# Performance work log

Hardware: AMD Instinct MI355X
Metric: run time of the kernel (lower is better)

## Reference

```python
import math
import jax, jax.numpy as jnp
import numpy as np

B, H, HW, C = 4, 8, 2048, 64
TEMPERATURE = 8.0  # sqrt(head_dim)
EPS = 0.5


def _l2norm(x, axis):
    return x / (1e-6 + jnp.linalg.norm(x, axis=axis, keepdims=True))


def setup_inputs() -> dict:
    key = jax.random.key(0)
    kq, kk, kv, ka = jax.random.split(key, 4)
    q = jax.random.normal(kq, (B, H, HW, C), dtype=jnp.float32)
    k = jax.random.normal(kk, (B, H, HW, C), dtype=jnp.float32)
    v = jax.random.normal(kv, (B, H, HW, C), dtype=jnp.float32)
    a_rand = jax.random.normal(ka, (B, H, HW, C), dtype=jnp.float32) * math.sqrt(2.0 / C)
    return {"q": q, "k": k, "v": v, "a_rand": a_rand}


def reference(q, k, v, a_rand):
    # Elementwise OT-style score modification of K
    k_l2 = _l2norm(k, -1)
    v_l2 = _l2norm(v, -1)
    kv_sim = jnp.clip(k_l2 * v_l2, 0.0, None)        # [B,H,HW,C]
    K_mat = jnp.exp(-(1.0 - kv_sim) / EPS)
    a = _l2norm(a_rand, 1)                            # normalize over heads dim
    b = k / K_mat * a
    a2 = v / K_mat * b
    k_updated = k * a2
    # Full N^2 attention with modified keys
    attn = jax.nn.softmax(
        jnp.einsum('bhqc,bhkc->bhqk', q / TEMPERATURE, k_updated), axis=-1
    )                                                 # [B,H,HW,HW]
    out = jnp.einsum('bhqk,bhkc->bhqc', attn, v)      # [B,H,HW,C]
    return out, attn
```

## Files before the change

kernel.cpp:

```cpp
#include <hip/hip_runtime.h>
#include <hip/hip_bf16.h>
#include <math.h>

#define B_ 4
#define H_ 8
#define N_ 2048
#define C_ 64
#define BM 64
#define BN 64
#define LDH 72

typedef _Float16 half8 __attribute__((ext_vector_type(8)));
typedef _Float16 half4 __attribute__((ext_vector_type(4)));
typedef float f32x4 __attribute__((ext_vector_type(4)));

#if __has_builtin(__builtin_amdgcn_exp2f)
#define EXP2(x) __builtin_amdgcn_exp2f(x)
#else
#define EXP2(x) exp2f(x)
#endif

__global__ __launch_bounds__(512) void prep_kernel(
    const float* __restrict__ k,
    const float* __restrict__ v,
    const float* __restrict__ a_rand,
    _Float16* __restrict__ kup_hi,
    _Float16* __restrict__ kup_lo)
{
    int bn = blockIdx.x;
    int b = bn >> 11, n = bn & (N_ - 1);
    int t = threadIdx.x;
    int h = t >> 6, c = t & 63;
    size_t idx = (((size_t)(b * H_ + h)) * N_ + n) * C_ + c;
    float kf = k[idx];
    float vf = v[idx];
    float af = a_rand[idx];
    float ks = kf * kf, vs = vf * vf;
    #pragma unroll
    for (int m = 1; m < 64; m <<= 1) {
        ks += __shfl_xor(ks, m, 64);
        vs += __shfl_xor(vs, m, 64);
    }
    float kinv = 1.0f / (1e-6f + sqrtf(ks));
    float vinv = 1.0f / (1e-6f + sqrtf(vs));
    __shared__ float a2s[H_][C_];
    a2s[h][c] = af * af;
    __syncthreads();
    float asum = 0.0f;
    #pragma unroll
    for (int hh = 0; hh < H_; hh++) asum += a2s[hh][c];
    float ainv = 1.0f / (1e-6f + sqrtf(asum));
    float s = fmaxf(kf * kinv * vf * vinv, 0.0f);
    float kupf = kf * kf * vf * (af * ainv) * EXP2(5.7707801635558535f * (1.0f - s));
    kupf = fminf(fmaxf(kupf, -60000.0f), 60000.0f);
    _Float16 hi = (_Float16)kupf;
    _Float16 lo = (_Float16)(kupf - (float)hi);
    kup_hi[idx] = hi;
    kup_lo[idx] = lo;
}

__global__ __launch_bounds__(256, 4) void attn_kernel(
    const float* __restrict__ q,
    const float* __restrict__ v,
    const _Float16* __restrict__ kup_hi,
    const _Float16* __restrict__ kup_lo,
    float* __restrict__ out,
    float* __restrict__ attn)
{
    __shared__ __align__(16) _Float16 KQh[BM * LDH];
    __shared__ __align__(16) _Float16 KQl[BM * LDH];
    __shared__ __align__(16) _Float16 Vt[C_ * LDH + 64];
    __shared__ __align__(16) _Float16 Ps[BM * LDH];

    int bh = blockIdx.x;
    int qb = blockIdx.y * BM;
    int t = threadIdx.x;
    int w = t >> 6, lane = t & 63;
    int quad = lane >> 4, lc = lane & 15;

    const size_t base = (size_t)bh * N_ * C_;
    const float* qg = q + base + (size_t)qb * C_;
    const _Float16* kgh = kup_hi + base;
    const _Float16* kgl = kup_lo + base;
    const float* vg = v + base;

    const float qscale = 0.18033688011112042f;
    #pragma unroll
    for (int it = 0; it < 4; it++) {
        int idx = it * 256 + t;
        int row = idx >> 4, seg = idx & 15;
        float4 d = *(const float4*)(qg + (size_t)row * C_ + seg * 4);
        float f0 = d.x * qscale, f1 = d.y * qscale, f2 = d.z * qscale, f3 = d.w * qscale;
        half4 hv, lv;
        hv[0] = (_Float16)f0; lv[0] = (_Float16)(f0 - (float)hv[0]);
        hv[1] = (_Float16)f1; lv[1] = (_Float16)(f1 - (float)hv[1]);
        hv[2] = (_Float16)f2; lv[2] = (_Float16)(f2 - (float)hv[2]);
        hv[3] = (_Float16)f3; lv[3] = (_Float16)(f3 - (float)hv[3]);
        *(half4*)&KQh[row * LDH + seg * 4] = hv;
        *(half4*)&KQl[row * LDH + seg * 4] = lv;
    }
    __syncthreads();

    half8 qa0 = *(half8*)&KQh[(w * 16 + lc) * LDH + 0 + quad * 8];
    half8 qa1 = *(half8*)&KQh[(w * 16 + lc) * LDH + 32 + quad * 8];
    half8 ql0 = *(half8*)&KQl[(w * 16 + lc) * LDH + 0 + quad * 8];
    half8 ql1 = *(half8*)&KQl[(w * 16 + lc) * LDH + 32 + quad * 8];

    float m_run[4], l_run[4];
    f32x4 Oacc[4];
    #pragma unroll
    for (int r = 0; r < 4; r++) { m_run[r] = -INFINITY; l_run[r] = 0.0f; }
    #pragma unroll
    for (int sc = 0; sc < 4; sc++) Oacc[sc] = (f32x4){0.f, 0.f, 0.f, 0.f};

    for (int j0 = 0; j0 < N_; j0 += BN) {
        __syncthreads();
        #pragma unroll
        for (int it = 0; it < 2; it++) {
            int idx = it * 256 + t;
            int row = idx >> 3, seg = idx & 7;
            *(half8*)&KQh[row * LDH + seg * 8] =
                *(const half8*)(kgh + (size_t)(j0 + row) * C_ + seg * 8);
            *(half8*)&KQl[row * LDH + seg * 8] =
                *(const half8*)(kgl + (size_t)(j0 + row) * C_ + seg * 8);
        }
        __syncthreads();
        f32x4 S[4];
        #pragma unroll
        for (int s = 0; s < 4; s++) {
            half8 bh0 = *(half8*)&KQh[(s * 16 + lc) * LDH + 0 + quad * 8];
            half8 bh1 = *(half8*)&KQh[(s * 16 + lc) * LDH + 32 + quad * 8];
            half8 bl0 = *(half8*)&KQl[(s * 16 + lc) * LDH + 0 + quad * 8];
            half8 bl1 = *(half8*)&KQl[(s * 16 + lc) * LDH + 32 + quad * 8];
            f32x4 acc = (f32x4){0.f, 0.f, 0.f, 0.f};
            acc = __builtin_amdgcn_mfma_f32_16x16x32_f16(qa0, bh0, acc, 0, 0, 0);
            acc = __builtin_amdgcn_mfma_f32_16x16x32_f16(qa1, bh1, acc, 0, 0, 0);
            acc = __builtin_amdgcn_mfma_f32_16x16x32_f16(qa0, bl0, acc, 0, 0, 0);
            acc = __builtin_amdgcn_mfma_f32_16x16x32_f16(qa1, bl1, acc, 0, 0, 0);
            acc = __builtin_amdgcn_mfma_f32_16x16x32_f16(ql0, bh0, acc, 0, 0, 0);
            acc = __builtin_amdgcn_mfma_f32_16x16x32_f16(ql1, bh1, acc, 0, 0, 0);
            S[s] = acc;
        }
        #pragma unroll
        for (int r = 0; r < 4; r++) {
            float mloc = fmaxf(fmaxf(S[0][r], S[1][r]), fmaxf(S[2][r], S[3][r]));
            float mnew = fmaxf(m_run[r], mloc);
            float rs = EXP2(S[0][r] - mnew) + EXP2(S[1][r] - mnew) +
                       EXP2(S[2][r] - mnew) + EXP2(S[3][r] - mnew);
            l_run[r] = l_run[r] * EXP2(m_run[r] - mnew) + rs;
            m_run[r] = mnew;
        }
    }
    #pragma unroll
    for (int r = 0; r < 4; r++) {
        float m = m_run[r], l = l_run[r];
        #pragma unroll
        for (int msk = 1; msk < 16; msk <<= 1) {
            float mo = __shfl_xor(m, msk, 64);
            float lo = __shfl_xor(l, msk, 64);
            float mn = fmaxf(m, mo);
            l = l * EXP2(m - mn) + lo * EXP2(mo - mn);
            m = mn;
        }
        m_run[r] = m;
        l_run[r] = 1.0f / l;
    }

    float* attng = attn + (size_t)bh * N_ * N_ + (size_t)qb * N_;

    for (int j0 = 0; j0 < N_; j0 += BN) {
        __syncthreads();
        #pragma unroll
        for (int it = 0; it < 2; it++) {
            int idx = it * 256 + t;
            int row = idx >> 3, seg = idx & 7;
            *(half8*)&KQh[row * LDH + seg * 8] =
                *(const half8*)(kgh + (size_t)(j0 + row) * C_ + seg * 8);
            *(half8*)&KQl[row * LDH + seg * 8] =
                *(const half8*)(kgl + (size_t)(j0 + row) * C_ + seg * 8);
        }
        {
            int key = t >> 2, cb = (t & 3) * 16;
            int ofs = (t & 3) * 16;
            const float* vr = vg + (size_t)(j0 + key) * C_ + cb;
            #pragma unroll
            for (int i = 0; i < 16; i += 4) {
                float4 d = *(const float4*)(vr + i);
                Vt[(cb + i + 0) * LDH + ofs + key] = (_Float16)d.x;
                Vt[(cb + i + 1) * LDH + ofs + key] = (_Float16)d.y;
                Vt[(cb + i + 2) * LDH + ofs + key] = (_Float16)d.z;
                Vt[(cb + i + 3) * LDH + ofs + key] = (_Float16)d.w;
            }
        }
        __syncthreads();
        f32x4 S[4];
        #pragma unroll
        for (int s = 0; s < 4; s++) {
            half8 bh0 = *(half8*)&KQh[(s * 16 + lc) * LDH + 0 + quad * 8];
            half8 bh1 = *(half8*)&KQh[(s * 16 + lc) * LDH + 32 + quad * 8];
            half8 bl0 = *(half8*)&KQl[(s * 16 + lc) * LDH + 0 + quad * 8];
            half8 bl1 = *(half8*)&KQl[(s * 16 + lc) * LDH + 32 + quad * 8];
            f32x4 acc = (f32x4){0.f, 0.f, 0.f, 0.f};
            acc = __builtin_amdgcn_mfma_f32_16x16x32_f16(qa0, bh0, acc, 0, 0, 0);
            acc = __builtin_amdgcn_mfma_f32_16x16x32_f16(qa1, bh1, acc, 0, 0, 0);
            acc = __builtin_amdgcn_mfma_f32_16x16x32_f16(qa0, bl0, acc, 0, 0, 0);
            acc = __builtin_amdgcn_mfma_f32_16x16x32_f16(qa1, bl1, acc, 0, 0, 0);
            acc = __builtin_amdgcn_mfma_f32_16x16x32_f16(ql0, bh0, acc, 0, 0, 0);
            acc = __builtin_amdgcn_mfma_f32_16x16x32_f16(ql1, bh1, acc, 0, 0, 0);
            S[s] = acc;
        }
        #pragma unroll
        for (int s = 0; s < 4; s++) {
            #pragma unroll
            for (int r = 0; r < 4; r++) {
                float p = EXP2(S[s][r] - m_run[r]) * l_run[r];
                Ps[(w * 16 + quad * 4 + r) * LDH + s * 16 + lc] = (_Float16)p;
            }
        }
        __syncthreads();
        #pragma unroll
        for (int kn = 0; kn < 2; kn++) {
            half8 pa = *(half8*)&Ps[(w * 16 + lc) * LDH + kn * 32 + quad * 8];
            #pragma unroll
            for (int sc = 0; sc < 4; sc++) {
                half8 vb = *(half8*)&Vt[(sc * 16 + lc) * LDH + sc * 16 + kn * 32 + quad * 8];
                Oacc[sc] = __builtin_amdgcn_mfma_f32_16x16x32_f16(pa, vb, Oacc[sc], 0, 0, 0);
            }
        }
        #pragma unroll
        for (int it = 0; it < 4; it++) {
            int idx = it * 256 + t;
            int row = idx >> 4, seg = idx & 15;
            half4 hv = *(half4*)&Ps[row * LDH + seg * 4];
            float4 o;
            o.x = (float)hv[0];
            o.y = (float)hv[1];
            o.z = (float)hv[2];
            o.w = (float)hv[3];
            *(float4*)(attng + (size_t)row * N_ + j0 + seg * 4) = o;
        }
    }

    float* og = out + base + (size_t)qb * C_;
    #pragma unroll
    for (int sc = 0; sc < 4; sc++) {
        #pragma unroll
        for (int r = 0; r < 4; r++) {
            og[(size_t)(w * 16 + quad * 4 + r) * C_ + sc * 16 + lc] = Oacc[sc][r];
        }
    }
}

extern "C" void kernel_launch(void* const* d_in, const int* in_sizes, int n_in,
                              void* d_out, int out_size, void* d_ws, size_t ws_size,
                              hipStream_t stream) {
    const float* q = (const float*)d_in[0];
    const float* k = (const float*)d_in[1];
    const float* v = (const float*)d_in[2];
    const float* a = (const float*)d_in[3];
    const size_t nelem = (size_t)B_ * H_ * N_ * C_;
    _Float16* kup_hi = (_Float16*)d_ws;
    _Float16* kup_lo = kup_hi + nelem;
    float* out = (float*)d_out;
    float* attn = out + nelem;

    prep_kernel<<<dim3(B_ * N_), dim3(512), 0, stream>>>(k, v, a, kup_hi, kup_lo);
    attn_kernel<<<dim3(B_ * H_, N_ / BM), dim3(256), 0, stream>>>(q, v, kup_hi, kup_lo, out, attn);
}
```

Measured before the change: 749.5 us.

## Pre-transpose V to fp16, register-prefetch K/V tiles, write attn directly from registers

Adds a separate kernel that converts V to fp16 and transposes it once, so the attention loop loads V tiles with plain vector copies instead of per-element transposed LDS stores. K hi/lo and V tiles for the next block are prefetched into registers while the current block is computed, overlapping global loads with MFMA work. The attention probabilities are now stored to global straight from registers in fp32, which removes one barrier and the LDS read-back pass, at the cost of narrower stores. The launch-bounds occupancy hint is lowered from 4 to 3 to make room for the extra prefetch registers, and the workspace needs an extra fp16 V buffer.

```diff
diff --git a/kernel.cpp b/kernel.cpp
--- a/kernel.cpp
+++ b/kernel.cpp
@@ -59,9 +59,39 @@
     kup_lo[idx] = lo;
 }
 
-__global__ __launch_bounds__(256, 4) void attn_kernel(
+__global__ __launch_bounds__(256) void transpose_v_kernel(
+    const float* __restrict__ v,
+    _Float16* __restrict__ vt)
+{
+    __shared__ _Float16 T[C_ * LDH];
+    int bh = blockIdx.x;
+    int n0 = blockIdx.y * 64;
+    int t = threadIdx.x;
+    {
+        int nl = t >> 2, cs = (t & 3) * 16;
+        const float* src = v + (size_t)bh * N_ * C_ + (size_t)(n0 + nl) * C_ + cs;
+        #pragma unroll
+        for (int i = 0; i < 16; i += 4) {
+            float4 d = *(const float4*)(src + i);
+            T[(cs + i + 0) * LDH + nl] = (_Float16)d.x;
+            T[(cs + i + 1) * LDH + nl] = (_Float16)d.y;
+            T[(cs + i + 2) * LDH + nl] = (_Float16)d.z;
+            T[(cs + i + 3) * LDH + nl] = (_Float16)d.w;
+        }
+    }
+    __syncthreads();
+    #pragma unroll
+    for (int it = 0; it < 2; it++) {
+        int idx = it * 256 + t;
+        int c = idx >> 3, seg = idx & 7;
+        *(half8*)(vt + (size_t)bh * C_ * N_ + (size_t)c * N_ + n0 + seg * 8) =
+            *(half8*)&T[c * LDH + seg * 8];
+    }
+}
+
+__global__ __launch_bounds__(256, 3) void attn_kernel(
     const float* __restrict__ q,
-    const float* __restrict__ v,
+    const _Float16* __restrict__ vt,
     const _Float16* __restrict__ kup_hi,
     const _Float16* __restrict__ kup_lo,
     float* __restrict__ out,
@@ -69,7 +99,7 @@
 {
     __shared__ __align__(16) _Float16 KQh[BM * LDH];
     __shared__ __align__(16) _Float16 KQl[BM * LDH];
-    __shared__ __align__(16) _Float16 Vt[C_ * LDH + 64];
+    __shared__ __align__(16) _Float16 Vt[C_ * LDH];
     __shared__ __align__(16) _Float16 Ps[BM * LDH];
 
     int bh = blockIdx.x;
@@ -82,7 +112,10 @@
     const float* qg = q + base + (size_t)qb * C_;
     const _Float16* kgh = kup_hi + base;
     const _Float16* kgl = kup_lo + base;
-    const float* vg = v + base;
+    const _Float16* vtg = vt + base;
+
+    const int r0 = t >> 3, r1 = 32 + (t >> 3);
+    const int s0 = (t & 7) * 8;
 
     const float qscale = 0.18033688011112042f;
     #pragma unroll
@@ -113,16 +146,23 @@
     #pragma unroll
     for (int sc = 0; sc < 4; sc++) Oacc[sc] = (f32x4){0.f, 0.f, 0.f, 0.f};
 
+    half8 pk0h, pk1h, pk0l, pk1l, pv0, pv1;
+    pk0h = *(const half8*)(kgh + (size_t)r0 * C_ + s0);
+    pk1h = *(const half8*)(kgh + (size_t)r1 * C_ + s0);
+    pk0l = *(const half8*)(kgl + (size_t)r0 * C_ + s0);
+    pk1l = *(const half8*)(kgl + (size_t)r1 * C_ + s0);
+
     for (int j0 = 0; j0 < N_; j0 += BN) {
         __syncthreads();
-        #pragma unroll
-        for (int it = 0; it < 2; it++) {
-            int idx = it * 256 + t;
-            int row = idx >> 3, seg = idx & 7;
-            *(half8*)&KQh[row * LDH + seg * 8] =
-                *(const half8*)(kgh + (size_t)(j0 + row) * C_ + seg * 8);
-            *(half8*)&KQl[row * LDH + seg * 8] =
-                *(const half8*)(kgl + (size_t)(j0 + row) * C_ + seg * 8);
+        *(half8*)&KQh[r0 * LDH + s0] = pk0h;
+        *(half8*)&KQh[r1 * LDH + s0] = pk1h;
+        *(half8*)&KQl[r0 * LDH + s0] = pk0l;
+        *(half8*)&KQl[r1 * LDH + s0] = pk1l;
+        if (j0 + BN < N_) {
+            pk0h = *(const half8*)(kgh + (size_t)(j0 + BN + r0) * C_ + s0);
+            pk1h = *(const half8*)(kgh + (size_t)(j0 + BN + r1) * C_ + s0);
+            pk0l = *(const half8*)(kgl + (size_t)(j0 + BN + r0) * C_ + s0);
+            pk1l = *(const half8*)(kgl + (size_t)(j0 + BN + r1) * C_ + s0);
         }
         __syncthreads();
         f32x4 S[4];
@@ -168,29 +208,28 @@
 
     float* attng = attn + (size_t)bh * N_ * N_ + (size_t)qb * N_;
 
+    pk0h = *(const half8*)(kgh + (size_t)r0 * C_ + s0);
+    pk1h = *(const half8*)(kgh + (size_t)r1 * C_ + s0);
+    pk0l = *(const half8*)(kgl + (size_t)r0 * C_ + s0);
+    pk1l = *(const half8*)(kgl + (size_t)r1 * C_ + s0);
+    pv0  = *(const half8*)(vtg + (size_t)r0 * N_ + s0);
+    pv1  = *(const half8*)(vtg + (size_t)r1 * N_ + s0);
+
     for (int j0 = 0; j0 < N_; j0 += BN) {
         __syncthreads();
-        #pragma unroll
-        for (int it = 0; it < 2; it++) {
-            int idx = it * 256 + t;
-            int row = idx >> 3, seg = idx & 7;
-            *(half8*)&KQh[row * LDH + seg * 8] =
-                *(const half8*)(kgh + (size_t)(j0 + row) * C_ + seg * 8);
-            *(half8*)&KQl[row * LDH + seg * 8] =
-                *(const half8*)(kgl + (size_t)(j0 + row) * C_ + seg * 8);
-        }
-        {
-            int key = t >> 2, cb = (t & 3) * 16;
-            int ofs = (t & 3) * 16;
-            const float* vr = vg + (size_t)(j0 + key) * C_ + cb;
-            #pragma unroll
-            for (int i = 0; i < 16; i += 4) {
-                float4 d = *(const float4*)(vr + i);
-                Vt[(cb + i + 0) * LDH + ofs + key] = (_Float16)d.x;
-                Vt[(cb + i + 1) * LDH + ofs + key] = (_Float16)d.y;
-                Vt[(cb + i + 2) * LDH + ofs + key] = (_Float16)d.z;
-                Vt[(cb + i + 3) * LDH + ofs + key] = (_Float16)d.w;
-            }
+        *(half8*)&KQh[r0 * LDH + s0] = pk0h;
+        *(half8*)&KQh[r1 * LDH + s0] = pk1h;
+        *(half8*)&KQl[r0 * LDH + s0] = pk0l;
+        *(half8*)&KQl[r1 * LDH + s0] = pk1l;
+        *(half8*)&Vt[r0 * LDH + s0] = pv0;
+        *(half8*)&Vt[r1 * LDH + s0] = pv1;
+        if (j0 + BN < N_) {
+            pk0h = *(const half8*)(kgh + (size_t)(j0 + BN + r0) * C_ + s0);
+            pk1h = *(const half8*)(kgh + (size_t)(j0 + BN + r1) * C_ + s0);
+            pk0l = *(const half8*)(kgl + (size_t)(j0 + BN + r0) * C_ + s0);
+            pk1l = *(const half8*)(kgl + (size_t)(j0 + BN + r1) * C_ + s0);
+            pv0  = *(const half8*)(vtg + (size_t)r0 * N_ + j0 + BN + s0);
+            pv1  = *(const half8*)(vtg + (size_t)r1 * N_ + j0 + BN + s0);
         }
         __syncthreads();
         f32x4 S[4];
@@ -214,30 +253,18 @@
             #pragma unroll
             for (int r = 0; r < 4; r++) {
                 float p = EXP2(S[s][r] - m_run[r]) * l_run[r];
+                attng[(size_t)(w * 16 + quad * 4 + r) * N_ + j0 + s * 16 + lc] = p;
                 Ps[(w * 16 + quad * 4 + r) * LDH + s * 16 + lc] = (_Float16)p;
             }
         }
-        __syncthreads();
         #pragma unroll
         for (int kn = 0; kn < 2; kn++) {
             half8 pa = *(half8*)&Ps[(w * 16 + lc) * LDH + kn * 32 + quad * 8];
             #pragma unroll
             for (int sc = 0; sc < 4; sc++) {
-                half8 vb = *(half8*)&Vt[(sc * 16 + lc) * LDH + sc * 16 + kn * 32 + quad * 8];
+                half8 vb = *(half8*)&Vt[(sc * 16 + lc) * LDH + kn * 32 + quad * 8];
                 Oacc[sc] = __builtin_amdgcn_mfma_f32_16x16x32_f16(pa, vb, Oacc[sc], 0, 0, 0);
             }
-        }
-        #pragma unroll
-        for (int it = 0; it < 4; it++) {
-            int idx = it * 256 + t;
-            int row = idx >> 4, seg = idx & 15;
-            half4 hv = *(half4*)&Ps[row * LDH + seg * 4];
-            float4 o;
-            o.x = (float)hv[0];
-            o.y = (float)hv[1];
-            o.z = (float)hv[2];
-            o.w = (float)hv[3];
-            *(float4*)(attng + (size_t)row * N_ + j0 + seg * 4) = o;
         }
     }
 
@@ -261,9 +288,11 @@
     const size_t nelem = (size_t)B_ * H_ * N_ * C_;
     _Float16* kup_hi = (_Float16*)d_ws;
     _Float16* kup_lo = kup_hi + nelem;
+    _Float16* vtb    = kup_lo + nelem;
     float* out = (float*)d_out;
     float* attn = out + nelem;
 
     prep_kernel<<<dim3(B_ * N_), dim3(512), 0, stream>>>(k, v, a, kup_hi, kup_lo);
-    attn_kernel<<<dim3(B_ * H_, N_ / BM), dim3(256), 0, stream>>>(q, v, kup_hi, kup_lo, out, attn);
-}
+    transpose_v_kernel<<<dim3(B_ * H_, N_ / 64), dim3(256), 0, stream>>>(v, vtb);
+    attn_kernel<<<dim3(B_ * H_, N_ / BM), dim3(256), 0, stream>>>(q, vtb, kup_hi, kup_lo, out, attn);
+}
```

After: 714.0 us. 1.05x faster.
